# Optimization experiments

Hardware: AMD Instinct MI355X
Metric: run time of the kernel (lower is better)

The kernel has to match this reference:

```python
import jax, jax.numpy as jnp
import numpy as np

DIM = 384
HEADS = 12
HEAD_DIM = DIM // HEADS
WIN = (2, 7, 7)
NW_TOK = WIN[0] * WIN[1] * WIN[2]  # 98
SCALE = HEAD_DIM ** -0.5


def _relative_position_index():
    d = np.arange(WIN[0]); h = np.arange(WIN[1]); w = np.arange(WIN[2])
    coords = np.stack(np.meshgrid(d, h, w, indexing='ij'))  # [3,D,H,W]
    cf = coords.reshape(3, -1)  # [3, NW_TOK]
    rel = cf[:, :, None] - cf[:, None, :]  # [3, N, N]
    rel = rel.transpose(1, 2, 0).astype(np.int64)
    rel[:, :, 0] += WIN[0] - 1
    rel[:, :, 1] += WIN[1] - 1
    rel[:, :, 2] += WIN[2] - 1
    rel[:, :, 0] *= (2 * WIN[1] - 1) * (2 * WIN[2] - 1)
    rel[:, :, 1] *= 2 * WIN[2] - 1
    return rel.sum(-1)  # [NW_TOK, NW_TOK]


def setup_inputs() -> dict:
    key = jax.random.key(0)
    ks = jax.random.split(key, 6)
    B_, N = 1024, NW_TOK + 1
    nW = 64
    table_len = (2 * WIN[0] - 1) * (2 * WIN[1] - 1) * (2 * WIN[2] - 1)  # 507
    x = jax.random.normal(ks[0], (B_, N, DIM), dtype=jnp.float32)
    mask = jax.random.normal(ks[1], (nW, NW_TOK, NW_TOK), dtype=jnp.float32)
    W_qkv = jax.random.normal(ks[2], (DIM, 3 * DIM), dtype=jnp.float32) * 0.02
    rpb_table = jax.random.normal(ks[3], (table_len, HEADS), dtype=jnp.float32) * 0.02
    W_proj = jax.random.normal(ks[4], (DIM, DIM), dtype=jnp.float32) * 0.02
    b_proj = jnp.zeros((DIM,), dtype=jnp.float32)
    rpi = jnp.asarray(_relative_position_index(), dtype=jnp.int32)
    return {"x": x, "mask": mask, "W_qkv": W_qkv, "rpb_table": rpb_table,
            "W_proj": W_proj, "b_proj": b_proj, "rpi": rpi}


def reference(x, mask, W_qkv, rpb_table, W_proj, b_proj, rpi):
    B_, N, C = x.shape
    qkv = (x @ W_qkv).reshape(B_, N, 3, HEADS, HEAD_DIM)
    q, k, v = qkv[:, :, 0], qkv[:, :, 1], qkv[:, :, 2]  # [B_, N, H, hd]
    attn = jnp.einsum('bnhd,bmhd->bhnm', q * SCALE, k)  # [B_, H, N, N]
    # gathered relative position bias over non-class tokens, zero-padded for class token
    bias = rpb_table[rpi.reshape(-1)].reshape(NW_TOK, NW_TOK, HEADS).transpose(2, 0, 1)
    bias_full = jnp.pad(bias, ((0, 0), (1, 0), (1, 0)))  # [H, N, N]
    attn = attn + bias_full[None]
    nW = mask.shape[0]
    mask_full = jnp.pad(mask, ((0, 0), (1, 0), (1, 0)))  # [nW, N, N]
    attn = attn.reshape(B_ // nW, nW, HEADS, N, N) + mask_full[None, :, None]
    attn = attn.reshape(B_, HEADS, N, N)
    attn = jax.nn.softmax(attn, axis=-1)
    out = jnp.einsum('bhnm,bmhd->bnhd', attn, v).reshape(B_, N, C)
    out = out @ W_proj + b_proj
    return out[:, 1:], out[:, :1]
```

## Files before the change

kernel.cpp:

```cpp
#include <hip/hip_runtime.h>
#include <hip/hip_bf16.h>
#include <cstddef>
#include <cstdint>


using bf16 = __hip_bfloat16;
typedef short v8s __attribute__((ext_vector_type(8)));
typedef short v4s __attribute__((ext_vector_type(4)));
typedef float v4f __attribute__((ext_vector_type(4)));

static constexpr int    NTOK   = 99;
static constexpr int    CDIM   = 384;
static constexpr int    NHEAD  = 12;
static constexpr int    NROWS  = 101376;
static constexpr size_t PLANE  = (size_t)NROWS * 32;
static constexpr float  SCALEF = 0.17677669529663687f;

__device__ __forceinline__ v4f mfma16x16x32(v8s a, v8s b, v4f c) {
  return __builtin_amdgcn_mfma_f32_16x16x32_bf16(a, b, c, 0, 0, 0);
}
__device__ __forceinline__ short f2bf(float f) {
  bf16 h = __float2bfloat16(f);
  return *reinterpret_cast<short*>(&h);
}
__device__ __forceinline__ float bf2f(short s) {
  bf16 h = *reinterpret_cast<bf16*>(&s);
  return __bfloat162float(h);
}

#if defined(__has_builtin)
#if __has_builtin(__builtin_amdgcn_global_load_lds)
#define HAS_GLL 1
#endif
#endif
#ifndef HAS_GLL
#define HAS_GLL 0
#endif

__device__ __forceinline__ void gload_lds16(const bf16* gsrc, bf16* ldst, int lane) {
#if HAS_GLL
  __builtin_amdgcn_global_load_lds(
      (const __attribute__((address_space(1))) void*)gsrc,
      (__attribute__((address_space(3))) void*)ldst, 16, 0, 0);
#else
  *(v8s*)(ldst + lane * 8) = *(const v8s*)gsrc;
#endif
}

static constexpr size_t WT_QKV_OFF = 0;
static constexpr size_t WT_P_OFF   = 884736;
static constexpr size_t BIAS_OFF   = 884736 + 294912;
static constexpr size_t COMMON_END = 1650096;
static constexpr size_t O_WS_OFF   = COMMON_END;
static constexpr size_t WS_MID     = O_WS_OFF + (size_t)NROWS * 384 * 2;
static constexpr size_t BMF_OFF    = COMMON_END;
static constexpr size_t BMF_BYTES  = (size_t)64 * NHEAD * 7 * 7 * 64 * 4 * 2;
static constexpr size_t QKV_OFF    = BMF_OFF + BMF_BYTES;
static constexpr size_t WS_FULL    = QKV_OFF + (size_t)NROWS * 1152 * 2;
static constexpr size_t XB_OFF     = WS_FULL;
static constexpr size_t WS_FULL2   = XB_OFF + (size_t)NROWS * 384 * 2;

static constexpr int PREP_BASE = 1152 * 384 + 384 * 384 + NHEAD * 99 * 99;
static constexpr int PREP_BMF2 = 64 * 112 * 112;
static constexpr int PREP_XB   = NROWS * 384 / 8;
static constexpr int BMF_BLKS  = (PREP_BMF2 + 511) / 512;

__device__ __forceinline__ void bmf_gen_item(int j2, const float* __restrict__ rpb,
                                             const int* __restrict__ rpi,
                                             const float* __restrict__ mask,
                                             bf16* __restrict__ BMF)
{
  int col = j2 % 112;
  int r2  = j2 / 112;
  int row = r2 % 112;
  int wi  = r2 / 112;
  int w = row >> 4, g = (row >> 2) & 3, jj = row & 3;
  int t = col >> 4, li = col & 15, lane = g * 16 + li;
  bool in = (row >= 1 && row <= 98 && col >= 1 && col <= 98);
  int tix = 0; float mval = 0.f;
  if (in) {
    tix  = rpi[(row - 1) * 98 + (col - 1)];
    mval = mask[((size_t)wi * 98 + (row - 1)) * 98 + (col - 1)];
  }
  size_t base = (((size_t)wi * NHEAD * 7 + w) * 7 + t) * 256 + lane * 4 + jj;
  #pragma unroll
  for (int h = 0; h < NHEAD; ++h) {
    float v;
    if (col > 98)  v = -1e30f;
    else           v = in ? (rpb[tix * NHEAD + h] + mval) : 0.f;
    BMF[base + (size_t)h * 12544] = __float2bfloat16(v);
  }
}

__global__ void prep_kernel(const float* __restrict__ Wqkv, const float* __restrict__ Wproj,
                            const float* __restrict__ rpb,  const int* __restrict__ rpi,
                            const float* __restrict__ mask, const float* __restrict__ x,
                            bf16* __restrict__ WtQKV, bf16* __restrict__ WtP,
                            float* __restrict__ BIAS, bf16* __restrict__ BMF,
                            bf16* __restrict__ xb, int do_bmf, int do_xb)
{
  int idx = blockIdx.x * 256 + threadIdx.x;
  if (idx < 1152 * 384) {
    int c = idx / 384, k = idx - c * 384;
    WtQKV[idx] = __float2bfloat16(Wqkv[k * 1152 + c]);
  } else if (idx < 1152 * 384 + 384 * 384) {
    int j = idx - 1152 * 384;
    int c = j / 384, k = j - c * 384;
    WtP[j] = __float2bfloat16(Wproj[k * 384 + c]);
  } else if (idx < PREP_BASE) {
    int j = idx - (1152 * 384 + 384 * 384);
    int h = j / (99 * 99), r = j % (99 * 99);
    int nn = r / 99, mm = r % 99;
    float v = 0.f;
    if (nn > 0 && mm > 0) v = rpb[rpi[(nn - 1) * 98 + (mm - 1)] * NHEAD + h];
    BIAS[j] = v;
  } else if (do_bmf && idx < PREP_BASE + PREP_BMF2) {
    bmf_gen_item(idx - PREP_BASE, rpb, rpi, mask, BMF);
  } else if (do_xb && idx >= PREP_BASE + PREP_BMF2 &&
             idx < PREP_BASE + PREP_BMF2 + PREP_XB) {
    int j3 = idx - (PREP_BASE + PREP_BMF2);
    size_t off = (size_t)j3 * 8;
    v4f x0 = *(const v4f*)(x + off);
    v4f x1 = *(const v4f*)(x + off + 4);
    v8s f;
    #pragma unroll
    for (int j = 0; j < 4; ++j) { f[j] = f2bf(x0[j]); f[j + 4] = f2bf(x1[j]); }
    *(v8s*)(xb + off) = f;
  }
}

static constexpr int Q2_BUF  = 40960;
static constexpr int Q2_AOFF = 24576;
static constexpr int CSTG1_LD = 200;

__global__ __launch_bounds__(512)
void k_qkv2(const bf16* __restrict__ xb, const bf16* __restrict__ WtQKV,
            bf16* __restrict__ qkv2,
            const float* __restrict__ rpb, const int* __restrict__ rpi,
            const float* __restrict__ mask, bf16* __restrict__ BMF)
{
  __shared__ __align__(16) char smem[2 * Q2_BUF];
  bf16* C_stg = (bf16*)(smem);

  if (blockIdx.x < BMF_BLKS) {
    int j2 = blockIdx.x * 512 + threadIdx.x;
    if (j2 < PREP_BMF2) bmf_gen_item(j2, rpb, rpi, mask, BMF);
    return;
  }
  const int bid  = blockIdx.x - BMF_BLKS;

  const int tid  = threadIdx.x;
  const int wave = tid >> 6;
  const int wm   = wave >> 2;
  const int wn   = wave & 3;
  const int lane = tid & 63;
  const int g    = lane >> 4;
  const int li   = lane & 15;
  const int tile = (bid & 7) * 594 + (bid >> 3);
  const int R0   = (tile / 6) * 128;
  const int CN   = (tile % 6) * 192;

  v4f acc[4][3];
  #pragma unroll
  for (int mi = 0; mi < 4; ++mi)
    #pragma unroll
    for (int ni = 0; ni < 3; ++ni) acc[mi][ni] = (v4f){0.f, 0.f, 0.f, 0.f};

  auto stage = [&](int kc, int buf) {
    const int k0 = kc * 64;
    bf16* Bl = (bf16*)(smem + buf * Q2_BUF);
    bf16* Al = (bf16*)(smem + buf * Q2_BUF + Q2_AOFF);
    #pragma unroll
    for (int p = 0; p < 3; ++p) {
      int q = wave * 3 + p;
      int row = q * 8 + (lane >> 3);
      int c = (lane & 7) ^ (row & 7);
      gload_lds16(WtQKV + (size_t)(CN + row) * 384 + k0 + c * 8, Bl + q * 512, lane);
    }
    #pragma unroll
    for (int p = 0; p < 2; ++p) {
      int q = wave * 2 + p;
      int row = q * 8 + (lane >> 3);
      int c = (lane & 7) ^ (row & 7);
      gload_lds16(xb + (size_t)(R0 + row) * 384 + k0 + c * 8, Al + q * 512, lane);
    }
  };

  stage(0, 0);
  for (int kc = 0; kc < 6; ++kc) {
    if (kc < 5) {
      stage(kc + 1, (kc + 1) & 1);
      asm volatile("s_waitcnt vmcnt(5)" ::: "memory");
    } else {
      asm volatile("s_waitcnt vmcnt(0)" ::: "memory");
    }
    __builtin_amdgcn_s_barrier();
    __builtin_amdgcn_sched_barrier(0);
    const bf16* Bl = (const bf16*)(smem + (kc & 1) * Q2_BUF);
    const bf16* Al = (const bf16*)(smem + (kc & 1) * Q2_BUF + Q2_AOFF);
    #pragma unroll
    for (int ks = 0; ks < 2; ++ks) {
      v8s af[4], bfr[3];
      #pragma unroll
      for (int mi = 0; mi < 4; ++mi) {
        int arow = wm * 64 + mi * 16 + li;
        int sc   = (4 * ks + g) ^ (arow & 7);
        af[mi] = *(const v8s*)(Al + arow * 64 + sc * 8);
      }
      #pragma unroll
      for (int ni = 0; ni < 3; ++ni) {
        int brow = wn * 48 + ni * 16 + li;
        int sc   = (4 * ks + g) ^ (brow & 7);
        bfr[ni] = *(const v8s*)(Bl + brow * 64 + sc * 8);
      }
      #pragma unroll
      for (int mi = 0; mi < 4; ++mi)
        #pragma unroll
        for (int ni = 0; ni < 3; ++ni)
          acc[mi][ni] = mfma16x16x32(af[mi], bfr[ni], acc[mi][ni]);
    }
    __builtin_amdgcn_sched_barrier(0);
    __builtin_amdgcn_s_barrier();
  }

  const float scale = (CN < 384) ? SCALEF : 1.f;
  #pragma unroll
  for (int mi = 0; mi < 4; ++mi)
    #pragma unroll
    for (int ni = 0; ni < 3; ++ni)
      #pragma unroll
      for (int j = 0; j < 4; ++j)
        C_stg[(wm * 64 + mi * 16 + g * 4 + j) * CSTG1_LD + wn * 48 + ni * 16 + li] =
            __float2bfloat16(acc[mi][ni][j] * scale);
  __syncthreads();
  const int r_ep = tid >> 2, d8 = tid & 3;
  #pragma unroll
  for (int cidx = 0; cidx < 6; ++cidx) {
    int c_global = CN + cidx * 32;
    int seg = c_global / 384, hh = (c_global % 384) >> 5;
    bf16* plane = qkv2 + (size_t)(hh * 3 + seg) * PLANE;
    v8s val = *(const v8s*)(C_stg + r_ep * CSTG1_LD + cidx * 32 + d8 * 8);
    *(v8s*)(plane + (size_t)(R0 + r_ep) * 32 + d8 * 8) = val;
  }
}

static constexpr int GQB_OFF  = 0;
static constexpr int GQA_OFF  = 24576;
static constexpr int GQ_LDS2  = GQA_OFF + 128 * 72 * 2;
static constexpr int CSTG_LD  = 104;

__global__ __launch_bounds__(512)
void k_qkv(const float* __restrict__ x, const bf16* __restrict__ WtQKV,
           bf16* __restrict__ qkv2)
{
  __shared__ __align__(16) char smem[GQ_LDS2];
  bf16* B_lds = (bf16*)(smem + GQB_OFF);
  bf16* A_lds = (bf16*)(smem + GQA_OFF);
  bf16* C_stg = (bf16*)(smem);

  const int tid  = threadIdx.x;
  const int wave = tid >> 6;
  const int wm   = wave >> 2;
  const int wn   = wave & 3;
  const int lane = tid & 63;
  const int g    = lane >> 4;
  const int li   = lane & 15;
  const int tile = (blockIdx.x & 7) * 594 + (blockIdx.x >> 3);
  const int R0   = (tile / 6) * 128;
  const int CN   = (tile % 6) * 192;

  const int arr = tid >> 3, ak8 = tid & 7;

  v4f acc[4][3];
  #pragma unroll
  for (int mi = 0; mi < 4; ++mi)
    #pragma unroll
    for (int ni = 0; ni < 3; ++ni) acc[mi][ni] = (v4f){0.f, 0.f, 0.f, 0.f};

  v4f areg[2][2];
  auto load_areg = [&](int kc) {
    const int k0 = kc * 64;
    #pragma unroll
    for (int p = 0; p < 2; ++p) {
      const float* src = x + (size_t)(R0 + arr + p * 64) * 384 + k0 + ak8 * 8;
      areg[p][0] = *(const v4f*)(src);
      areg[p][1] = *(const v4f*)(src + 4);
    }
  };
  auto write_alds = [&]() {
    #pragma unroll
    for (int p = 0; p < 2; ++p) {
      v8s f;
      #pragma unroll
      for (int j = 0; j < 4; ++j) { f[j] = f2bf(areg[p][0][j]); f[j + 4] = f2bf(areg[p][1][j]); }
      *(v8s*)(A_lds + (arr + p * 64) * 72 + ak8 * 8) = f;
    }
  };

  load_areg(0);

  for (int kc = 0; kc < 6; ++kc) {
    const int k0 = kc * 64;
    write_alds();
    #pragma unroll
    for (int p = 0; p < 3; ++p) {
      int q   = wave * 3 + p;
      int row = q * 8 + (lane >> 3);
      int c   = (lane & 7) ^ (row & 7);
      const bf16* gsrc = WtQKV + (size_t)(CN + row) * 384 + k0 + c * 8;
      gload_lds16(gsrc, B_lds + q * 512, lane);
    }
    if (kc < 5) load_areg(kc + 1);
    __syncthreads();
    #pragma unroll
    for (int ks = 0; ks < 2; ++ks) {
      v8s af[4], bfr[3];
      #pragma unroll
      for (int mi = 0; mi < 4; ++mi)
        af[mi] = *(const v8s*)(A_lds + (wm * 64 + mi * 16 + li) * 72 + ks * 32 + g * 8);
      #pragma unroll
      for (int ni = 0; ni < 3; ++ni) {
        int brow = wn * 48 + ni * 16 + li;
        int sc   = (g + 4 * ks) ^ (brow & 7);
        bfr[ni]  = *(const v8s*)(B_lds + brow * 64 + sc * 8);
      }
      #pragma unroll
      for (int mi = 0; mi < 4; ++mi)
        #pragma unroll
        for (int ni = 0; ni < 3; ++ni)
          acc[mi][ni] = mfma16x16x32(af[mi], bfr[ni], acc[mi][ni]);
    }
    __syncthreads();
  }

  const float scale = (CN < 384) ? SCALEF : 1.f;
  const int r_ep = tid >> 2, d8 = tid & 3;
  #pragma unroll
  for (int half = 0; half < 2; ++half) {
    __syncthreads();
    if ((wn >> 1) == half) {
      #pragma unroll
      for (int mi = 0; mi < 4; ++mi)
        #pragma unroll
        for (int ni = 0; ni < 3; ++ni)
          #pragma unroll
          for (int j = 0; j < 4; ++j)
            C_stg[(wm * 64 + mi * 16 + g * 4 + j) * CSTG_LD + (wn & 1) * 48 + ni * 16 + li] =
                __float2bfloat16(acc[mi][ni][j] * scale);
    }
    __syncthreads();
    #pragma unroll
    for (int cidx = 0; cidx < 3; ++cidx) {
      int c_global = CN + half * 96 + cidx * 32;
      int seg = c_global / 384, hh = (c_global % 384) >> 5;
      bf16* plane = qkv2 + (size_t)(hh * 3 + seg) * PLANE;
      v8s val = *(const v8s*)(C_stg + r_ep * CSTG_LD + cidx * 32 + d8 * 8);
      *(v8s*)(plane + (size_t)(R0 + r_ep) * 32 + d8 * 8) = val;
    }
  }
}

static constexpr int A_VT_LD = 136;
static constexpr int A_P_LD  = 136;
static constexpr int A_OFF_V = 0;
static constexpr int A_OFF_P = A_OFF_V + 32 * A_VT_LD * 2;
static constexpr int A_LDS   = A_OFF_P + 112 * A_P_LD * 2;

__global__ __launch_bounds__(448)
void k_attn(const bf16* __restrict__ BMF, bf16* __restrict__ qkv2)
{
  __shared__ __align__(16) char smem[A_LDS];
  bf16* vT_lds = (bf16*)(smem + A_OFF_V);
  bf16* P_lds  = (bf16*)(smem + A_OFF_P);

  const int b    = blockIdx.x;
  const int tid  = threadIdx.x;
  const int wave = tid >> 6;
  const int lane = tid & 63;
  const int g    = lane >> 4;
  const int li   = lane & 15;
  const int wi   = b & 63;

  const int r = tid >> 2, l4 = tid & 3;
  const size_t voff = ((size_t)b * NTOK + ((r > 98) ? 98 : r)) * 32 + l4 * 8;

  const int qrow = (16 * wave + li > 98) ? 98 : 16 * wave + li;
  const size_t qoff = ((size_t)b * NTOK + qrow) * 32 + g * 8;
  int koff[7];
  #pragma unroll
  for (int t = 0; t < 7; ++t) {
    int krow = 16 * t + li; if (krow > 98) krow = 98;
    koff[t] = (b * NTOK + krow) * 32 + g * 8;
  }
  const bf16* bmw = BMF + ((size_t)(wi * NHEAD) * 7 + wave) * 7 * 256 + lane * 4;

  v8s pv = *(const v8s*)(qkv2 + (size_t)2 * PLANE + voff);

  for (int z = tid; z < A_LDS / 16; z += 448)
    *(v8s*)(smem + z * 16) = (v8s){0, 0, 0, 0, 0, 0, 0, 0};
  __syncthreads();

  if (r < NTOK) {
    #pragma unroll
    for (int e = 0; e < 8; ++e)
      *(short*)(vT_lds + (l4 * 8 + e) * A_VT_LD + r) = pv[e];
  }

  v8s kf[7], qf;
  v4s bmr[7];
  {
    const bf16* kp = qkv2 + (size_t)1 * PLANE;
    #pragma unroll
    for (int t = 0; t < 7; ++t) kf[t] = *(const v8s*)(kp + koff[t]);
    qf = *(const v8s*)(qkv2 + qoff);
    #pragma unroll
    for (int t = 0; t < 7; ++t)
      bmr[t] = *(const v4s*)(bmw + t * 256);
  }
  __syncthreads();

  for (int h = 0; h < NHEAD; ++h) {
    v4f sacc[7];
    #pragma unroll
    for (int t = 0; t < 7; ++t) {
      v4f z = (v4f){0.f, 0.f, 0.f, 0.f};
      sacc[t] = mfma16x16x32(qf, kf[t], z);
    }

    v8s nv;
    if (h < NHEAD - 1) {
      const bf16* kp = qkv2 + (size_t)((h + 1) * 3 + 1) * PLANE;
      #pragma unroll
      for (int t = 0; t < 7; ++t) kf[t] = *(const v8s*)(kp + koff[t]);
      qf = *(const v8s*)(qkv2 + (size_t)((h + 1) * 3) * PLANE + qoff);
      nv = *(const v8s*)(qkv2 + (size_t)((h + 1) * 3 + 2) * PLANE + voff);
    }

    #pragma unroll
    for (int t = 0; t < 7; ++t)
      #pragma unroll
      for (int j = 0; j < 4; ++j)
        sacc[t][j] += bf2f(bmr[t][j]);

    if (h < NHEAD - 1) {
      const bf16* bmb = bmw + (size_t)(h + 1) * 12544;
      #pragma unroll
      for (int t = 0; t < 7; ++t)
        bmr[t] = *(const v4s*)(bmb + t * 256);
    }

    float linv[4];
    #pragma unroll
    for (int j = 0; j < 4; ++j) {
      float m = -1e30f;
      #pragma unroll
      for (int t = 0; t < 7; ++t) m = fmaxf(m, sacc[t][j]);
      m = fmaxf(m, __shfl_xor(m, 1));
      m = fmaxf(m, __shfl_xor(m, 2));
      m = fmaxf(m, __shfl_xor(m, 4));
      m = fmaxf(m, __shfl_xor(m, 8));
      float l = 0.f;
      #pragma unroll
      for (int t = 0; t < 7; ++t) {
        float p = __expf(sacc[t][j] - m);
        sacc[t][j] = p;
        l += p;
      }
      l += __shfl_xor(l, 1);
      l += __shfl_xor(l, 2);
      l += __shfl_xor(l, 4);
      l += __shfl_xor(l, 8);
      linv[j] = 1.f / l;
      int row = 16 * wave + g * 4 + j;
      #pragma unroll
      for (int t = 0; t < 7; ++t)
        P_lds[row * A_P_LD + 16 * t + li] = __float2bfloat16(sacc[t][j]);
    }
    v4f oacc[2];
    oacc[0] = (v4f){0.f, 0.f, 0.f, 0.f};
    oacc[1] = (v4f){0.f, 0.f, 0.f, 0.f};
    #pragma unroll
    for (int ks = 0; ks < 4; ++ks) {
      v8s ap = *(const v8s*)(P_lds + (16 * wave + li) * A_P_LD + ks * 32 + g * 8);
      #pragma unroll
      for (int t = 0; t < 2; ++t) {
        v8s bv = *(const v8s*)(vT_lds + (16 * t + li) * A_VT_LD + ks * 32 + g * 8);
        oacc[t] = mfma16x16x32(ap, bv, oacc[t]);
      }
    }
    bf16* oplane = qkv2 + (size_t)(h * 3) * PLANE;
    #pragma unroll
    for (int t = 0; t < 2; ++t)
      #pragma unroll
      for (int j = 0; j < 4; ++j) {
        int row = 16 * wave + g * 4 + j;
        if (row < NTOK)
          oplane[((size_t)b * NTOK + row) * 32 + 16 * t + li] =
              __float2bfloat16(oacc[t][j] * linv[j]);
      }

    asm volatile("s_waitcnt lgkmcnt(0)" ::: "memory");
    asm volatile("s_barrier" ::: "memory");
    if (h < NHEAD - 1) {
      if (r < NTOK) {
        #pragma unroll
        for (int e = 0; e < 8; ++e)
          *(short*)(vT_lds + (l4 * 8 + e) * A_VT_LD + r) = nv[e];
      }
      asm volatile("s_waitcnt lgkmcnt(0)" ::: "memory");
      asm volatile("s_barrier" ::: "memory");
    }
  }
}

__global__ __launch_bounds__(512)
void k2_proj2(const bf16* __restrict__ O_src, const bf16* __restrict__ WtP,
              const float* __restrict__ bproj, float* __restrict__ out)
{
  __shared__ __align__(16) char smem[2 * Q2_BUF];

  const int tid  = threadIdx.x;
  const int wave = tid >> 6;
  const int wm   = wave >> 2;
  const int wn   = wave & 3;
  const int lane = tid & 63;
  const int g    = lane >> 4;
  const int li   = lane & 15;
  const int tile = (blockIdx.x & 7) * 198 + (blockIdx.x >> 3);
  const int R0   = (tile >> 1) * 128;
  const int CN   = (tile & 1) * 192;

  v4f acc[4][3];
  #pragma unroll
  for (int mi = 0; mi < 4; ++mi)
    #pragma unroll
    for (int ni = 0; ni < 3; ++ni) acc[mi][ni] = (v4f){0.f, 0.f, 0.f, 0.f};

  auto stage = [&](int kc, int buf) {
    const int k0 = kc * 64;
    bf16* Wl = (bf16*)(smem + buf * Q2_BUF);
    bf16* Ol = (bf16*)(smem + buf * Q2_BUF + Q2_AOFF);
    #pragma unroll
    for (int p = 0; p < 3; ++p) {
      int q = wave * 3 + p;
      int row = q * 8 + (lane >> 3);
      int c = (lane & 7) ^ (row & 7);
      gload_lds16(WtP + (size_t)(CN + row) * CDIM + k0 + c * 8, Wl + q * 512, lane);
    }
    #pragma unroll
    for (int p = 0; p < 2; ++p) {
      int q = wave * 2 + p;
      int row = q * 8 + (lane >> 3);
      int c = (lane & 7) ^ (row & 7);
      int kk = k0 + c * 8, hh = kk >> 5, d = kk & 31;
      gload_lds16(O_src + (size_t)(hh * 3) * PLANE + (size_t)(R0 + row) * 32 + d,
                  Ol + q * 512, lane);
    }
  };

  stage(0, 0);
  for (int kc = 0; kc < 6; ++kc) {
    if (kc < 5) {
      stage(kc + 1, (kc + 1) & 1);
      asm volatile("s_waitcnt vmcnt(5)" ::: "memory");
    } else {
      asm volatile("s_waitcnt vmcnt(0)" ::: "memory");
    }
    __builtin_amdgcn_s_barrier();
    __builtin_amdgcn_sched_barrier(0);
    const bf16* Wl = (const bf16*)(smem + (kc & 1) * Q2_BUF);
    const bf16* Ol = (const bf16*)(smem + (kc & 1) * Q2_BUF + Q2_AOFF);
    #pragma unroll
    for (int ks = 0; ks < 2; ++ks) {
      v8s af[4], bfr[3];
      #pragma unroll
      for (int mi = 0; mi < 4; ++mi) {
        int arow = wm * 64 + mi * 16 + li;
        int sc   = (4 * ks + g) ^ (arow & 7);
        af[mi] = *(const v8s*)(Ol + arow * 64 + sc * 8);
      }
      #pragma unroll
      for (int ni = 0; ni < 3; ++ni) {
        int brow = wn * 48 + ni * 16 + li;
        int sc   = (4 * ks + g) ^ (brow & 7);
        bfr[ni] = *(const v8s*)(Wl + brow * 64 + sc * 8);
      }
      #pragma unroll
      for (int mi = 0; mi < 4; ++mi)
        #pragma unroll
        for (int ni = 0; ni < 3; ++ni)
          acc[mi][ni] = mfma16x16x32(af[mi], bfr[ni], acc[mi][ni]);
    }
    __builtin_amdgcn_sched_barrier(0);
    __builtin_amdgcn_s_barrier();
  }

  const size_t OUT2 = (size_t)1024 * 98 * CDIM;
  #pragma unroll
  for (int mi = 0; mi < 4; ++mi)
    #pragma unroll
    for (int ni = 0; ni < 3; ++ni) {
      int col = CN + wn * 48 + ni * 16 + li;
      float bb = bproj[col];
      #pragma unroll
      for (int j = 0; j < 4; ++j) {
        int rr = R0 + wm * 64 + mi * 16 + g * 4 + j;
        int b = rr / 99, n = rr - b * 99;
        float v = acc[mi][ni][j] + bb;
        if (n == 0) out[OUT2 + (size_t)b * CDIM + col] = v;
        else        out[((size_t)b * 98 + (n - 1)) * CDIM + col] = v;
      }
    }
}

static constexpr int K2_LD   = 72;
static constexpr int K2_OFFW = 0;
static constexpr int K2_OFFO = 192 * K2_LD * 2;
static constexpr int K2_LDS  = K2_OFFO + 128 * K2_LD * 2;

__global__ __launch_bounds__(512)
void k2_proj(const bf16* __restrict__ O_src, const bf16* __restrict__ WtP,
             const float* __restrict__ bproj, float* __restrict__ out)
{
  __shared__ __align__(16) char smem[K2_LDS];
  bf16* W_lds = (bf16*)(smem + K2_OFFW);
  bf16* O_lds = (bf16*)(smem + K2_OFFO);

  const int tid  = threadIdx.x;
  const int wave = tid >> 6;
  const int wm   = wave >> 2;
  const int wn   = wave & 3;
  const int lane = tid & 63;
  const int g    = lane >> 4;
  const int li   = lane & 15;
  const int tile = (blockIdx.x & 7) * 198 + (blockIdx.x >> 3);
  const int R0   = (tile >> 1) * 128;
  const int CN   = (tile & 1) * 192;

  v4f acc[4][3];
  #pragma unroll
  for (int mi = 0; mi < 4; ++mi)
    #pragma unroll
    for (int ni = 0; ni < 3; ++ni) acc[mi][ni] = (v4f){0.f, 0.f, 0.f, 0.f};

  for (int kc = 0; kc < 6; ++kc) {
    const int k0 = kc * 64;
    #pragma unroll
    for (int p = 0; p < 3; ++p) {
      int it = tid + p * 512, rr = it >> 3, k8 = it & 7;
      *(v8s*)(W_lds + rr * K2_LD + k8 * 8) =
          *(const v8s*)(WtP + (size_t)(CN + rr) * CDIM + k0 + k8 * 8);
    }
    #pragma unroll
    for (int p = 0; p < 2; ++p) {
      int it = tid + p * 512, rr = it >> 3, k8 = it & 7;
      *(v8s*)(O_lds + rr * K2_LD + k8 * 8) =
          *(const v8s*)(O_src + (size_t)(R0 + rr) * 384 + k0 + k8 * 8);
    }
    __syncthreads();
    #pragma unroll
    for (int ks = 0; ks < 2; ++ks) {
      v8s af[4], bfr[3];
      #pragma unroll
      for (int mi = 0; mi < 4; ++mi)
        af[mi] = *(const v8s*)(O_lds + (wm * 64 + mi * 16 + li) * K2_LD + ks * 32 + g * 8);
      #pragma unroll
      for (int ni = 0; ni < 3; ++ni)
        bfr[ni] = *(const v8s*)(W_lds + (wn * 48 + ni * 16 + li) * K2_LD + ks * 32 + g * 8);
      #pragma unroll
      for (int mi = 0; mi < 4; ++mi)
        #pragma unroll
        for (int ni = 0; ni < 3; ++ni)
          acc[mi][ni] = mfma16x16x32(af[mi], bfr[ni], acc[mi][ni]);
    }
    __syncthreads();
  }

  const size_t OUT2 = (size_t)1024 * 98 * CDIM;
  #pragma unroll
  for (int mi = 0; mi < 4; ++mi)
    #pragma unroll
    for (int ni = 0; ni < 3; ++ni) {
      int col = CN + wn * 48 + ni * 16 + li;
      float bb = bproj[col];
      #pragma unroll
      for (int j = 0; j < 4; ++j) {
        int rr = R0 + wm * 64 + mi * 16 + g * 4 + j;
        int b = rr / 99, n = rr - b * 99;
        float v = acc[mi][ni][j] + bb;
        if (n == 0) out[OUT2 + (size_t)b * CDIM + col] = v;
        else        out[((size_t)b * 98 + (n - 1)) * CDIM + col] = v;
      }
    }
}

static constexpr int QK_LD = 40;
static constexpr int VT_LD = 136;
static constexpr int P_LD  = 136;
static constexpr int WS_LD = 104;
static constexpr int K1_OFF_Q = 0;
static constexpr int K1_OFF_K = K1_OFF_Q + 112 * QK_LD * 2;
static constexpr int K1_OFF_V = K1_OFF_K + 112 * QK_LD * 2;
static constexpr int K1_OFF_P = K1_OFF_V + 32  * VT_LD * 2;
static constexpr int K1_OFF_W = K1_OFF_P + 112 * P_LD  * 2;
static constexpr int K1_LDS   = K1_OFF_W + 96 * WS_LD * 2;

__global__ __launch_bounds__(512)
void k1_attn(const float* __restrict__ x, const float* __restrict__ mask,
             const float* __restrict__ BIAS, const bf16* __restrict__ WtQKV,
             bf16* __restrict__ O_ws)
{
  __shared__ __align__(16) char smem[K1_LDS];
  bf16* q_lds  = (bf16*)(smem + K1_OFF_Q);
  bf16* k_lds  = (bf16*)(smem + K1_OFF_K);
  bf16* vT_lds = (bf16*)(smem + K1_OFF_V);
  bf16* P_lds  = (bf16*)(smem + K1_OFF_P);
  bf16* w_lds  = (bf16*)(smem + K1_OFF_W);

  const int b    = blockIdx.x;
  const int tid  = threadIdx.x;
  const int wave = tid >> 6;
  const int lane = tid & 63;
  const int g    = lane >> 4;
  const int li   = lane & 15;
  const int wi   = b & 63;

  v8s afr[12];
  if (wave < 7) {
    int arow = 16 * wave + li; if (arow > 98) arow = 98;
    const float* xb = x + ((size_t)b * NTOK + arow) * CDIM + g * 8;
    #pragma unroll
    for (int s = 0; s < 12; ++s) {
      v4f x0 = *(const v4f*)(xb + s * 32);
      v4f x1 = *(const v4f*)(xb + s * 32 + 4);
      v8s f;
      #pragma unroll
      for (int j = 0; j < 4; ++j) { f[j] = f2bf(x0[j]); f[j + 4] = f2bf(x1[j]); }
      afr[s] = f;
    }
  }

  for (int h = 0; h < NHEAD; ++h) {
    v4f qacc[6];
    #pragma unroll
    for (int t = 0; t < 6; ++t) qacc[t] = (v4f){0.f, 0.f, 0.f, 0.f};
    #pragma unroll
    for (int c4 = 0; c4 < 4; ++c4) {
      for (int idx = tid; idx < 96 * 12; idx += 512) {
        int rr = idx / 12, ch = idx - rr * 12;
        int cg = (rr < 32) ? (h * 32 + rr)
               : (rr < 64) ? (CDIM + h * 32 + rr - 32)
                           : (2 * CDIM + h * 32 + rr - 64);
        *(v8s*)(w_lds + rr * WS_LD + ch * 8) =
            *(const v8s*)(WtQKV + (size_t)cg * CDIM + c4 * 96 + ch * 8);
      }
      __syncthreads();
      if (wave < 7) {
        #pragma unroll
        for (int ss = 0; ss < 3; ++ss) {
          const int s = c4 * 3 + ss;
          #pragma unroll
          for (int t = 0; t < 6; ++t) {
            v8s bw = *(const v8s*)(w_lds + (16 * t + li) * WS_LD + ss * 32 + g * 8);
            qacc[t] = mfma16x16x32(afr[s], bw, qacc[t]);
          }
        }
      }
      __syncthreads();
    }
    if (wave < 7) {
      #pragma unroll
      for (int t = 0; t < 6; ++t) {
        #pragma unroll
        for (int j = 0; j < 4; ++j) {
          int row = 16 * wave + g * 4 + j;
          int col = 16 * (t & 1) + li;
          float v = qacc[t][j];
          if (t < 2)      q_lds[row * QK_LD + col] = __float2bfloat16(v * SCALEF);
          else if (t < 4) k_lds[row * QK_LD + col] = __float2bfloat16(v);
          else            vT_lds[col * VT_LD + row] = __float2bfloat16(v);
        }
      }
    }
    vT_lds[(tid >> 4) * VT_LD + 112 + (tid & 15)] = __float2bfloat16(0.f);
    __syncthreads();

    if (wave < 7) {
      v8s aq = *(const v8s*)(q_lds + (16 * wave + li) * QK_LD + g * 8);
      v4f sacc[7];
      #pragma unroll
      for (int t = 0; t < 7; ++t) {
        v8s bk = *(const v8s*)(k_lds + (16 * t + li) * QK_LD + g * 8);
        v4f z = (v4f){0.f, 0.f, 0.f, 0.f};
        sacc[t] = mfma16x16x32(aq, bk, z);
      }
      #pragma unroll
      for (int t = 0; t < 7; ++t) {
        int col = 16 * t + li;
        #pragma unroll
        for (int j = 0; j < 4; ++j) {
          int row = 16 * wave + g * 4 + j;
          float s = sacc[t][j];
          if (col >= NTOK) s = -1e30f;
          else if (row < NTOK) {
            s += BIAS[(h * NTOK + row) * NTOK + col];
            if (row > 0 && col > 0)
              s += mask[((size_t)wi * 98 + (row - 1)) * 98 + (col - 1)];
          }
          sacc[t][j] = s;
        }
      }
      float linv[4];
      #pragma unroll
      for (int j = 0; j < 4; ++j) {
        float m = -1e30f;
        #pragma unroll
        for (int t = 0; t < 7; ++t) m = fmaxf(m, sacc[t][j]);
        m = fmaxf(m, __shfl_xor(m, 1));
        m = fmaxf(m, __shfl_xor(m, 2));
        m = fmaxf(m, __shfl_xor(m, 4));
        m = fmaxf(m, __shfl_xor(m, 8));
        float l = 0.f;
        #pragma unroll
        for (int t = 0; t < 7; ++t) {
          float p = __expf(sacc[t][j] - m);
          sacc[t][j] = p;
          l += p;
        }
        l += __shfl_xor(l, 1);
        l += __shfl_xor(l, 2);
        l += __shfl_xor(l, 4);
        l += __shfl_xor(l, 8);
        linv[j] = 1.f / l;
        int row = 16 * wave + g * 4 + j;
        #pragma unroll
        for (int t = 0; t < 7; ++t)
          P_lds[row * P_LD + 16 * t + li] = __float2bfloat16(sacc[t][j]);
        P_lds[row * P_LD + 112 + li] = __float2bfloat16(0.f);
      }
      v4f oacc[2];
      oacc[0] = (v4f){0.f, 0.f, 0.f, 0.f};
      oacc[1] = (v4f){0.f, 0.f, 0.f, 0.f};
      #pragma unroll
      for (int ks = 0; ks < 4; ++ks) {
        v8s ap = *(const v8s*)(P_lds + (16 * wave + li) * P_LD + ks * 32 + g * 8);
        #pragma unroll
        for (int t = 0; t < 2; ++t) {
          v8s bv = *(const v8s*)(vT_lds + (16 * t + li) * VT_LD + ks * 32 + g * 8);
          oacc[t] = mfma16x16x32(ap, bv, oacc[t]);
        }
      }
      #pragma unroll
      for (int t = 0; t < 2; ++t) {
        #pragma unroll
        for (int j = 0; j < 4; ++j) {
          int row = 16 * wave + g * 4 + j;
          if (row < NTOK)
            O_ws[((size_t)b * 99 + row) * CDIM + h * 32 + 16 * t + li] =
                __float2bfloat16(oacc[t][j] * linv[j]);
        }
      }
    }
    __syncthreads();
  }
}

static constexpr int M_O_LD = 392;
static constexpr int M_OFF_O = 0;
static constexpr int M_OFF_Q = M_OFF_O + 99  * M_O_LD * 2;
static constexpr int M_OFF_K = M_OFF_Q + 112 * QK_LD * 2;
static constexpr int M_OFF_V = M_OFF_K + 112 * QK_LD * 2;
static constexpr int M_OFF_P = M_OFF_V + 32  * VT_LD * 2;
static constexpr int M_OFF_W = M_OFF_P + 112 * P_LD  * 2;
static constexpr int M_LDS   = M_OFF_W + 96 * WS_LD * 2;

__global__ __launch_bounds__(512)
void fused_mono(const float* __restrict__ x, const float* __restrict__ mask,
                const float* __restrict__ bproj, const float* __restrict__ BIAS,
                const bf16* __restrict__ WtQKV, const bf16* __restrict__ WtP,
                float* __restrict__ out)
{
  __shared__ __align__(16) char smem[M_LDS];
  bf16* O_lds  = (bf16*)(smem + M_OFF_O);
  bf16* q_lds  = (bf16*)(smem + M_OFF_Q);
  bf16* k_lds  = (bf16*)(smem + M_OFF_K);
  bf16* vT_lds = (bf16*)(smem + M_OFF_V);
  bf16* P_lds  = (bf16*)(smem + M_OFF_P);
  bf16* w_lds  = (bf16*)(smem + M_OFF_W);

  const int b    = blockIdx.x;
  const int tid  = threadIdx.x;
  const int wave = tid >> 6;
  const int lane = tid & 63;
  const int g    = lane >> 4;
  const int li   = lane & 15;
  const int wi   = b & 63;

  v8s afr[12];
  if (wave < 7) {
    int arow = 16 * wave + li; if (arow > 98) arow = 98;
    const float* xb = x + ((size_t)b * NTOK + arow) * CDIM + g * 8;
    #pragma unroll
    for (int s = 0; s < 12; ++s) {
      v4f x0 = *(const v4f*)(xb + s * 32);
      v4f x1 = *(const v4f*)(xb + s * 32 + 4);
      v8s f;
      #pragma unroll
      for (int j = 0; j < 4; ++j) { f[j] = f2bf(x0[j]); f[j + 4] = f2bf(x1[j]); }
      afr[s] = f;
    }
  }

  for (int h = 0; h < NHEAD; ++h) {
    v4f qacc[6];
    #pragma unroll
    for (int t = 0; t < 6; ++t) qacc[t] = (v4f){0.f, 0.f, 0.f, 0.f};
    #pragma unroll
    for (int c4 = 0; c4 < 4; ++c4) {
      for (int idx = tid; idx < 96 * 12; idx += 512) {
        int rr = idx / 12, ch = idx - rr * 12;
        int cg = (rr < 32) ? (h * 32 + rr)
               : (rr < 64) ? (CDIM + h * 32 + rr - 32)
                           : (2 * CDIM + h * 32 + rr - 64);
        *(v8s*)(w_lds + rr * WS_LD + ch * 8) =
            *(const v8s*)(WtQKV + (size_t)cg * CDIM + c4 * 96 + ch * 8);
      }
      __syncthreads();
      if (wave < 7) {
        #pragma unroll
        for (int ss = 0; ss < 3; ++ss) {
          const int s = c4 * 3 + ss;
          #pragma unroll
          for (int t = 0; t < 6; ++t) {
            v8s bw = *(const v8s*)(w_lds + (16 * t + li) * WS_LD + ss * 32 + g * 8);
            qacc[t] = mfma16x16x32(afr[s], bw, qacc[t]);
          }
        }
      }
      __syncthreads();
    }
    if (wave < 7) {
      #pragma unroll
      for (int t = 0; t < 6; ++t) {
        #pragma unroll
        for (int j = 0; j < 4; ++j) {
          int row = 16 * wave + g * 4 + j;
          int col = 16 * (t & 1) + li;
          float v = qacc[t][j];
          if (t < 2)      q_lds[row * QK_LD + col] = __float2bfloat16(v * SCALEF);
          else if (t < 4) k_lds[row * QK_LD + col] = __float2bfloat16(v);
          else            vT_lds[col * VT_LD + row] = __float2bfloat16(v);
        }
      }
    }
    vT_lds[(tid >> 4) * VT_LD + 112 + (tid & 15)] = __float2bfloat16(0.f);
    __syncthreads();

    if (wave < 7) {
      v8s aq = *(const v8s*)(q_lds + (16 * wave + li) * QK_LD + g * 8);
      v4f sacc[7];
      #pragma unroll
      for (int t = 0; t < 7; ++t) {
        v8s bk = *(const v8s*)(k_lds + (16 * t + li) * QK_LD + g * 8);
        v4f z = (v4f){0.f, 0.f, 0.f, 0.f};
        sacc[t] = mfma16x16x32(aq, bk, z);
      }
      #pragma unroll
      for (int t = 0; t < 7; ++t) {
        int col = 16 * t + li;
        #pragma unroll
        for (int j = 0; j < 4; ++j) {
          int row = 16 * wave + g * 4 + j;
          float s = sacc[t][j];
          if (col >= NTOK) s = -1e30f;
          else if (row < NTOK) {
            s += BIAS[(h * NTOK + row) * NTOK + col];
            if (row > 0 && col > 0)
              s += mask[((size_t)wi * 98 + (row - 1)) * 98 + (col - 1)];
          }
          sacc[t][j] = s;
        }
      }
      float linv[4];
      #pragma unroll
      for (int j = 0; j < 4; ++j) {
        float m = -1e30f;
        #pragma unroll
        for (int t = 0; t < 7; ++t) m = fmaxf(m, sacc[t][j]);
        m = fmaxf(m, __shfl_xor(m, 1));
        m = fmaxf(m, __shfl_xor(m, 2));
        m = fmaxf(m, __shfl_xor(m, 4));
        m = fmaxf(m, __shfl_xor(m, 8));
        float l = 0.f;
        #pragma unroll
        for (int t = 0; t < 7; ++t) {
          float p = __expf(sacc[t][j] - m);
          sacc[t][j] = p;
          l += p;
        }
        l += __shfl_xor(l, 1);
        l += __shfl_xor(l, 2);
        l += __shfl_xor(l, 4);
        l += __shfl_xor(l, 8);
        linv[j] = 1.f / l;
        int row = 16 * wave + g * 4 + j;
        #pragma unroll
        for (int t = 0; t < 7; ++t)
          P_lds[row * P_LD + 16 * t + li] = __float2bfloat16(sacc[t][j]);
        P_lds[row * P_LD + 112 + li] = __float2bfloat16(0.f);
      }
      v4f oacc[2];
      oacc[0] = (v4f){0.f, 0.f, 0.f, 0.f};
      oacc[1] = (v4f){0.f, 0.f, 0.f, 0.f};
      #pragma unroll
      for (int ks = 0; ks < 4; ++ks) {
        v8s ap = *(const v8s*)(P_lds + (16 * wave + li) * P_LD + ks * 32 + g * 8);
        #pragma unroll
        for (int t = 0; t < 2; ++t) {
          v8s bv = *(const v8s*)(vT_lds + (16 * t + li) * VT_LD + ks * 32 + g * 8);
          oacc[t] = mfma16x16x32(ap, bv, oacc[t]);
        }
      }
      #pragma unroll
      for (int t = 0; t < 2; ++t) {
        #pragma unroll
        for (int j = 0; j < 4; ++j) {
          int row = 16 * wave + g * 4 + j;
          if (row < NTOK)
            O_lds[row * M_O_LD + h * 32 + 16 * t + li] =
                __float2bfloat16(oacc[t][j] * linv[j]);
        }
      }
    }
    __syncthreads();
  }

  const size_t OUT2 = (size_t)1024 * 98 * CDIM;
  const int orow_clamped = (16 * wave + li > 98) ? 98 : 16 * wave + li;
  for (int cc = 0; cc < 4; ++cc) {
    v4f pacc[6];
    #pragma unroll
    for (int t = 0; t < 6; ++t) pacc[t] = (v4f){0.f, 0.f, 0.f, 0.f};
    for (int c4 = 0; c4 < 4; ++c4) {
      for (int idx = tid; idx < 96 * 12; idx += 512) {
        int rr = idx / 12, ch = idx - rr * 12;
        *(v8s*)(w_lds + rr * WS_LD + ch * 8) =
            *(const v8s*)(WtP + ((size_t)(cc * 96 + rr)) * CDIM + c4 * 96 + ch * 8);
      }
      __syncthreads();
      if (wave < 7) {
        #pragma unroll
        for (int ss = 0; ss < 3; ++ss) {
          const int s = c4 * 3 + ss;
          v8s ao = *(const v8s*)(O_lds + orow_clamped * M_O_LD + s * 32 + g * 8);
          #pragma unroll
          for (int t = 0; t < 6; ++t) {
            v8s bw = *(const v8s*)(w_lds + (16 * t + li) * WS_LD + ss * 32 + g * 8);
            pacc[t] = mfma16x16x32(ao, bw, pacc[t]);
          }
        }
      }
      __syncthreads();
    }
    if (wave < 7) {
      #pragma unroll
      for (int t = 0; t < 6; ++t) {
        #pragma unroll
        for (int j = 0; j < 4; ++j) {
          int row = 16 * wave + g * 4 + j;
          if (row < NTOK) {
            int col = cc * 96 + 16 * t + li;
            float v = pacc[t][j] + bproj[col];
            if (row == 0) out[OUT2 + (size_t)b * CDIM + col] = v;
            else          out[((size_t)b * 98 + (row - 1)) * CDIM + col] = v;
          }
        }
      }
    }
  }
}

extern "C" void kernel_launch(void* const* d_in, const int* in_sizes, int n_in,
                              void* d_out, int out_size, void* d_ws, size_t ws_size,
                              hipStream_t stream) {
  const float* x     = (const float*)d_in[0];
  const float* mask  = (const float*)d_in[1];
  const float* Wqkv  = (const float*)d_in[2];
  const float* rpb   = (const float*)d_in[3];
  const float* Wproj = (const float*)d_in[4];
  const float* bproj = (const float*)d_in[5];
  const int*   rpi   = (const int*)d_in[6];

  bf16*  WtQKV = (bf16*)((char*)d_ws + WT_QKV_OFF);
  bf16*  WtP   = (bf16*)((char*)d_ws + WT_P_OFF);
  float* BIAS  = (float*)((char*)d_ws + BIAS_OFF);
  bf16*  BMF   = (bf16*)((char*)d_ws + BMF_OFF);
  bf16*  xbuf  = (bf16*)((char*)d_ws + XB_OFF);

  const bool full2 = (ws_size >= WS_FULL2);
  const bool full  = (ws_size >= WS_FULL);
  const int do_bmf_prep = (full && !full2) ? 1 : 0;
  int prep_items = PREP_BASE;
  if (do_bmf_prep) prep_items += PREP_BMF2;
  if (full2)       prep_items = PREP_BASE + PREP_BMF2 + PREP_XB;
  prep_kernel<<<(prep_items + 255) / 256, 256, 0, stream>>>(
      Wqkv, Wproj, rpb, rpi, mask, x, WtQKV, WtP, BIAS, BMF, xbuf,
      do_bmf_prep, full2 ? 1 : 0);

  if (full) {
    bf16* qkv2 = (bf16*)((char*)d_ws + QKV_OFF);
    if (full2)
      k_qkv2<<<BMF_BLKS + 792 * 6, 512, 0, stream>>>(xbuf, WtQKV, qkv2,
                                                     rpb, rpi, mask, BMF);
    else
      k_qkv<<<792 * 6, 512, 0, stream>>>(x, WtQKV, qkv2);
    k_attn<<<1024, 448, 0, stream>>>(BMF, qkv2);
    k2_proj2<<<792 * 2, 512, 0, stream>>>(qkv2, WtP, bproj, (float*)d_out);
  } else if (ws_size >= WS_MID) {
    bf16* O_ws = (bf16*)((char*)d_ws + O_WS_OFF);
    k1_attn<<<1024, 512, 0, stream>>>(x, mask, BIAS, WtQKV, O_ws);
    k2_proj<<<792 * 2, 512, 0, stream>>>(O_ws, WtP, bproj, (float*)d_out);
  } else {
    fused_mono<<<1024, 512, 0, stream>>>(x, mask, bproj, BIAS, WtQKV, WtP,
                                         (float*)d_out);
  }
}
```

Baseline: 403.2 us.

## Fuse fp32-to-bf16 conversion of x into QKV GEMM register-staged A loads

Drops the separate bf16 copy of x that the prep kernel wrote to workspace. The QKV GEMM now loads fp32 x into registers, converts it and writes swizzled bf16 tiles into LDS, double-buffered next to the async B loads. This avoids a full extra write and read of the activation, and the prep kernel skips bias generation when the full path is taken. In exchange the GEMM's A loads become register round-trips with extra waits instead of direct global-to-LDS copies, and each block reads twice as many A bytes.

```diff
diff --git a/kernel.cpp b/kernel.cpp
--- a/kernel.cpp
+++ b/kernel.cpp
@@ -57,12 +57,10 @@
 static constexpr size_t BMF_BYTES  = (size_t)64 * NHEAD * 7 * 7 * 64 * 4 * 2;
 static constexpr size_t QKV_OFF    = BMF_OFF + BMF_BYTES;
 static constexpr size_t WS_FULL    = QKV_OFF + (size_t)NROWS * 1152 * 2;
-static constexpr size_t XB_OFF     = WS_FULL;
-static constexpr size_t WS_FULL2   = XB_OFF + (size_t)NROWS * 384 * 2;
-
-static constexpr int PREP_BASE = 1152 * 384 + 384 * 384 + NHEAD * 99 * 99;
+
+static constexpr int PREP_W    = 1152 * 384 + 384 * 384;
+static constexpr int PREP_BASE = PREP_W + NHEAD * 99 * 99;
 static constexpr int PREP_BMF2 = 64 * 112 * 112;
-static constexpr int PREP_XB   = NROWS * 384 / 8;
 static constexpr int BMF_BLKS  = (PREP_BMF2 + 511) / 512;
 
 __device__ __forceinline__ void bmf_gen_item(int j2, const float* __restrict__ rpb,
@@ -94,38 +92,24 @@
 
 __global__ void prep_kernel(const float* __restrict__ Wqkv, const float* __restrict__ Wproj,
                             const float* __restrict__ rpb,  const int* __restrict__ rpi,
-                            const float* __restrict__ mask, const float* __restrict__ x,
                             bf16* __restrict__ WtQKV, bf16* __restrict__ WtP,
-                            float* __restrict__ BIAS, bf16* __restrict__ BMF,
-                            bf16* __restrict__ xb, int do_bmf, int do_xb)
+                            float* __restrict__ BIAS, int do_bias)
 {
   int idx = blockIdx.x * 256 + threadIdx.x;
   if (idx < 1152 * 384) {
     int c = idx / 384, k = idx - c * 384;
     WtQKV[idx] = __float2bfloat16(Wqkv[k * 1152 + c]);
-  } else if (idx < 1152 * 384 + 384 * 384) {
+  } else if (idx < PREP_W) {
     int j = idx - 1152 * 384;
     int c = j / 384, k = j - c * 384;
     WtP[j] = __float2bfloat16(Wproj[k * 384 + c]);
-  } else if (idx < PREP_BASE) {
-    int j = idx - (1152 * 384 + 384 * 384);
+  } else if (do_bias && idx < PREP_BASE) {
+    int j = idx - PREP_W;
     int h = j / (99 * 99), r = j % (99 * 99);
     int nn = r / 99, mm = r % 99;
     float v = 0.f;
     if (nn > 0 && mm > 0) v = rpb[rpi[(nn - 1) * 98 + (mm - 1)] * NHEAD + h];
     BIAS[j] = v;
-  } else if (do_bmf && idx < PREP_BASE + PREP_BMF2) {
-    bmf_gen_item(idx - PREP_BASE, rpb, rpi, mask, BMF);
-  } else if (do_xb && idx >= PREP_BASE + PREP_BMF2 &&
-             idx < PREP_BASE + PREP_BMF2 + PREP_XB) {
-    int j3 = idx - (PREP_BASE + PREP_BMF2);
-    size_t off = (size_t)j3 * 8;
-    v4f x0 = *(const v4f*)(x + off);
-    v4f x1 = *(const v4f*)(x + off + 4);
-    v8s f;
-    #pragma unroll
-    for (int j = 0; j < 4; ++j) { f[j] = f2bf(x0[j]); f[j + 4] = f2bf(x1[j]); }
-    *(v8s*)(xb + off) = f;
   }
 }
 
@@ -134,7 +118,7 @@
 static constexpr int CSTG1_LD = 200;
 
 __global__ __launch_bounds__(512)
-void k_qkv2(const bf16* __restrict__ xb, const bf16* __restrict__ WtQKV,
+void k_qkv2(const float* __restrict__ x, const bf16* __restrict__ WtQKV,
             bf16* __restrict__ qkv2,
             const float* __restrict__ rpb, const int* __restrict__ rpi,
             const float* __restrict__ mask, bf16* __restrict__ BMF)
@@ -160,16 +144,28 @@
   const int R0   = (tile / 6) * 128;
   const int CN   = (tile % 6) * 192;
 
+  const int arr = tid >> 3, ak8 = tid & 7;
+  const int alc = ak8 ^ (arr & 7);
+
   v4f acc[4][3];
   #pragma unroll
   for (int mi = 0; mi < 4; ++mi)
     #pragma unroll
     for (int ni = 0; ni < 3; ++ni) acc[mi][ni] = (v4f){0.f, 0.f, 0.f, 0.f};
 
-  auto stage = [&](int kc, int buf) {
+  v4f areg[2][2];
+  auto loadA = [&](int kc) {
+    const int k0 = kc * 64;
+    #pragma unroll
+    for (int p = 0; p < 2; ++p) {
+      const float* src = x + (size_t)(R0 + arr + p * 64) * 384 + k0 + ak8 * 8;
+      areg[p][0] = *(const v4f*)(src);
+      areg[p][1] = *(const v4f*)(src + 4);
+    }
+  };
+  auto loadB = [&](int kc, int buf) {
     const int k0 = kc * 64;
     bf16* Bl = (bf16*)(smem + buf * Q2_BUF);
-    bf16* Al = (bf16*)(smem + buf * Q2_BUF + Q2_AOFF);
     #pragma unroll
     for (int p = 0; p < 3; ++p) {
       int q = wave * 3 + p;
@@ -177,22 +173,32 @@
       int c = (lane & 7) ^ (row & 7);
       gload_lds16(WtQKV + (size_t)(CN + row) * 384 + k0 + c * 8, Bl + q * 512, lane);
     }
+  };
+  auto writeA = [&](int buf) {
+    bf16* Al = (bf16*)(smem + buf * Q2_BUF + Q2_AOFF);
     #pragma unroll
     for (int p = 0; p < 2; ++p) {
-      int q = wave * 2 + p;
-      int row = q * 8 + (lane >> 3);
-      int c = (lane & 7) ^ (row & 7);
-      gload_lds16(xb + (size_t)(R0 + row) * 384 + k0 + c * 8, Al + q * 512, lane);
+      v8s f;
+      #pragma unroll
+      for (int j = 0; j < 4; ++j) { f[j] = f2bf(areg[p][0][j]); f[j + 4] = f2bf(areg[p][1][j]); }
+      *(v8s*)(Al + (arr + p * 64) * 64 + alc * 8) = f;
     }
   };
 
-  stage(0, 0);
+  loadA(0);
+  loadB(0, 0);
+  asm volatile("s_waitcnt vmcnt(3)" ::: "memory");
+  writeA(0);
+
   for (int kc = 0; kc < 6; ++kc) {
     if (kc < 5) {
-      stage(kc + 1, (kc + 1) & 1);
-      asm volatile("s_waitcnt vmcnt(5)" ::: "memory");
+      loadA(kc + 1);
+      loadB(kc + 1, (kc + 1) & 1);
+      asm volatile("s_waitcnt vmcnt(3)" ::: "memory");
+      writeA((kc + 1) & 1);
+      asm volatile("s_waitcnt lgkmcnt(0)" ::: "memory");
     } else {
-      asm volatile("s_waitcnt vmcnt(0)" ::: "memory");
+      asm volatile("s_waitcnt vmcnt(0) lgkmcnt(0)" ::: "memory");
     }
     __builtin_amdgcn_s_barrier();
     __builtin_amdgcn_sched_barrier(0);
@@ -203,9 +209,9 @@
       v8s af[4], bfr[3];
       #pragma unroll
       for (int mi = 0; mi < 4; ++mi) {
-        int arow = wm * 64 + mi * 16 + li;
-        int sc   = (4 * ks + g) ^ (arow & 7);
-        af[mi] = *(const v8s*)(Al + arow * 64 + sc * 8);
+        int arow2 = wm * 64 + mi * 16 + li;
+        int sc    = (4 * ks + g) ^ (arow2 & 7);
+        af[mi] = *(const v8s*)(Al + arow2 * 64 + sc * 8);
       }
       #pragma unroll
       for (int ni = 0; ni < 3; ++ni) {
@@ -241,122 +247,6 @@
     bf16* plane = qkv2 + (size_t)(hh * 3 + seg) * PLANE;
     v8s val = *(const v8s*)(C_stg + r_ep * CSTG1_LD + cidx * 32 + d8 * 8);
     *(v8s*)(plane + (size_t)(R0 + r_ep) * 32 + d8 * 8) = val;
-  }
-}
-
-static constexpr int GQB_OFF  = 0;
-static constexpr int GQA_OFF  = 24576;
-static constexpr int GQ_LDS2  = GQA_OFF + 128 * 72 * 2;
-static constexpr int CSTG_LD  = 104;
-
-__global__ __launch_bounds__(512)
-void k_qkv(const float* __restrict__ x, const bf16* __restrict__ WtQKV,
-           bf16* __restrict__ qkv2)
-{
-  __shared__ __align__(16) char smem[GQ_LDS2];
-  bf16* B_lds = (bf16*)(smem + GQB_OFF);
-  bf16* A_lds = (bf16*)(smem + GQA_OFF);
-  bf16* C_stg = (bf16*)(smem);
-
-  const int tid  = threadIdx.x;
-  const int wave = tid >> 6;
-  const int wm   = wave >> 2;
-  const int wn   = wave & 3;
-  const int lane = tid & 63;
-  const int g    = lane >> 4;
-  const int li   = lane & 15;
-  const int tile = (blockIdx.x & 7) * 594 + (blockIdx.x >> 3);
-  const int R0   = (tile / 6) * 128;
-  const int CN   = (tile % 6) * 192;
-
-  const int arr = tid >> 3, ak8 = tid & 7;
-
-  v4f acc[4][3];
-  #pragma unroll
-  for (int mi = 0; mi < 4; ++mi)
-    #pragma unroll
-    for (int ni = 0; ni < 3; ++ni) acc[mi][ni] = (v4f){0.f, 0.f, 0.f, 0.f};
-
-  v4f areg[2][2];
-  auto load_areg = [&](int kc) {
-    const int k0 = kc * 64;
-    #pragma unroll
-    for (int p = 0; p < 2; ++p) {
-      const float* src = x + (size_t)(R0 + arr + p * 64) * 384 + k0 + ak8 * 8;
-      areg[p][0] = *(const v4f*)(src);
-      areg[p][1] = *(const v4f*)(src + 4);
-    }
-  };
-  auto write_alds = [&]() {
-    #pragma unroll
-    for (int p = 0; p < 2; ++p) {
-      v8s f;
-      #pragma unroll
-      for (int j = 0; j < 4; ++j) { f[j] = f2bf(areg[p][0][j]); f[j + 4] = f2bf(areg[p][1][j]); }
-      *(v8s*)(A_lds + (arr + p * 64) * 72 + ak8 * 8) = f;
-    }
-  };
-
-  load_areg(0);
-
-  for (int kc = 0; kc < 6; ++kc) {
-    const int k0 = kc * 64;
-    write_alds();
-    #pragma unroll
-    for (int p = 0; p < 3; ++p) {
-      int q   = wave * 3 + p;
-      int row = q * 8 + (lane >> 3);
-      int c   = (lane & 7) ^ (row & 7);
-      const bf16* gsrc = WtQKV + (size_t)(CN + row) * 384 + k0 + c * 8;
-      gload_lds16(gsrc, B_lds + q * 512, lane);
-    }
-    if (kc < 5) load_areg(kc + 1);
-    __syncthreads();
-    #pragma unroll
-    for (int ks = 0; ks < 2; ++ks) {
-      v8s af[4], bfr[3];
-      #pragma unroll
-      for (int mi = 0; mi < 4; ++mi)
-        af[mi] = *(const v8s*)(A_lds + (wm * 64 + mi * 16 + li) * 72 + ks * 32 + g * 8);
-      #pragma unroll
-      for (int ni = 0; ni < 3; ++ni) {
-        int brow = wn * 48 + ni * 16 + li;
-        int sc   = (g + 4 * ks) ^ (brow & 7);
-        bfr[ni]  = *(const v8s*)(B_lds + brow * 64 + sc * 8);
-      }
-      #pragma unroll
-      for (int mi = 0; mi < 4; ++mi)
-        #pragma unroll
-        for (int ni = 0; ni < 3; ++ni)
-          acc[mi][ni] = mfma16x16x32(af[mi], bfr[ni], acc[mi][ni]);
-    }
-    __syncthreads();
-  }
-
-  const float scale = (CN < 384) ? SCALEF : 1.f;
-  const int r_ep = tid >> 2, d8 = tid & 3;
-  #pragma unroll
-  for (int half = 0; half < 2; ++half) {
-    __syncthreads();
-    if ((wn >> 1) == half) {
-      #pragma unroll
-      for (int mi = 0; mi < 4; ++mi)
-        #pragma unroll
-        for (int ni = 0; ni < 3; ++ni)
-          #pragma unroll
-          for (int j = 0; j < 4; ++j)
-            C_stg[(wm * 64 + mi * 16 + g * 4 + j) * CSTG_LD + (wn & 1) * 48 + ni * 16 + li] =
-                __float2bfloat16(acc[mi][ni][j] * scale);
-    }
-    __syncthreads();
-    #pragma unroll
-    for (int cidx = 0; cidx < 3; ++cidx) {
-      int c_global = CN + half * 96 + cidx * 32;
-      int seg = c_global / 384, hh = (c_global % 384) >> 5;
-      bf16* plane = qkv2 + (size_t)(hh * 3 + seg) * PLANE;
-      v8s val = *(const v8s*)(C_stg + r_ep * CSTG_LD + cidx * 32 + d8 * 8);
-      *(v8s*)(plane + (size_t)(R0 + r_ep) * 32 + d8 * 8) = val;
-    }
   }
 }
 
@@ -1095,25 +985,16 @@
   bf16*  WtP   = (bf16*)((char*)d_ws + WT_P_OFF);
   float* BIAS  = (float*)((char*)d_ws + BIAS_OFF);
   bf16*  BMF   = (bf16*)((char*)d_ws + BMF_OFF);
-  bf16*  xbuf  = (bf16*)((char*)d_ws + XB_OFF);
-
-  const bool full2 = (ws_size >= WS_FULL2);
-  const bool full  = (ws_size >= WS_FULL);
-  const int do_bmf_prep = (full && !full2) ? 1 : 0;
-  int prep_items = PREP_BASE;
-  if (do_bmf_prep) prep_items += PREP_BMF2;
-  if (full2)       prep_items = PREP_BASE + PREP_BMF2 + PREP_XB;
+
+  const bool full = (ws_size >= WS_FULL);
+  const int prep_items = full ? PREP_W : PREP_BASE;
   prep_kernel<<<(prep_items + 255) / 256, 256, 0, stream>>>(
-      Wqkv, Wproj, rpb, rpi, mask, x, WtQKV, WtP, BIAS, BMF, xbuf,
-      do_bmf_prep, full2 ? 1 : 0);
+      Wqkv, Wproj, rpb, rpi, WtQKV, WtP, BIAS, full ? 0 : 1);
 
   if (full) {
     bf16* qkv2 = (bf16*)((char*)d_ws + QKV_OFF);
-    if (full2)
-      k_qkv2<<<BMF_BLKS + 792 * 6, 512, 0, stream>>>(xbuf, WtQKV, qkv2,
-                                                     rpb, rpi, mask, BMF);
-    else
-      k_qkv<<<792 * 6, 512, 0, stream>>>(x, WtQKV, qkv2);
+    k_qkv2<<<BMF_BLKS + 792 * 6, 512, 0, stream>>>(x, WtQKV, qkv2,
+                                                   rpb, rpi, mask, BMF);
     k_attn<<<1024, 448, 0, stream>>>(BMF, qkv2);
     k2_proj2<<<792 * 2, 512, 0, stream>>>(qkv2, WtP, bproj, (float*)d_out);
   } else if (ws_size >= WS_MID) {
```

Result: faster. 378.4 us (median of 3 runs) (-6.2%).
